# Performance work log

Hardware: AMD Instinct MI355X
Metric: run time of the kernel (lower is better)

## Reference

```python
import jax, jax.numpy as jnp
import numpy as np


def setup_inputs() -> dict:
    key = jax.random.key(0)
    k1, k2, k3, k4, k5 = jax.random.split(key, 5)
    B, Cin, H, W = 16, 64, 224, 224
    Cout, KH, KW = 64, 3, 3
    PH = PW = 32
    in_tensor = jax.random.normal(k1, (B, Cin, H, W), jnp.float32)
    weights = jax.random.normal(k2, (Cout, Cin, KH, KW), jnp.float32) * 0.05
    biases = jax.random.normal(k3, (Cout,), jnp.float32)
    # stale output buffer from a previous full conv; patch regions get overwritten
    out_tensor = jax.random.normal(k4, (B, Cout, H, W), jnp.float32)
    patch_location_tensor = jax.random.randint(k5, (B, 2), 0, H - PH, dtype=jnp.int32)
    return {
        "in_tensor": in_tensor,
        "weights": weights,
        "biases": biases,
        "out_tensor": out_tensor,
        "patch_location_tensor": patch_location_tensor,
        "padding": 1,
        "stride": 1,
        "p_height": PH,
        "p_width": PW,
        "version": 3,
    }


def reference(in_tensor, weights, biases, out_tensor, patch_location_tensor,
              padding, stride, p_height, p_width, version):
    KH, KW = weights.shape[2], weights.shape[3]
    Cin = in_tensor.shape[1]
    # pad once so output coord oy reads padded-input rows oy*stride .. oy*stride+KH-1
    xp = jnp.pad(in_tensor, ((0, 0), (0, 0), (padding, padding), (padding, padding)))
    if version in (1, 2):
        # full dense conv (versions 1/2)
        y = jax.lax.conv_general_dilated(xp, weights, (stride, stride), "VALID")
        return y + biases[None, :, None, None]
    # versions 3/4: compute conv only over the patch region, write into out buffer
    in_ph = (p_height - 1) * stride + KH  # input rows needed for PH output rows
    in_pw = (p_width - 1) * stride + KW

    def update_one(xpb, ob, loc):
        # xpb: (Cin, Hp, Wp), ob: (Cout, H, W), loc: (2,) = (y, x) in output coords
        region = jax.lax.dynamic_slice(
            xpb, (0, loc[0] * stride, loc[1] * stride), (Cin, in_ph, in_pw))
        patch = jax.lax.conv_general_dilated(
            region[None], weights, (stride, stride), "VALID")[0]
        patch = patch + biases[:, None, None]  # (Cout, PH, PW)
        return jax.lax.dynamic_update_slice(ob, patch, (0, loc[0], loc[1]))

    return jax.vmap(update_one)(xp, out_tensor, patch_location_tensor)
```

## Files before the change

### kernel.cpp

```cpp
#include <hip/hip_runtime.h>

constexpr int B_ = 16, C_ = 64, H_ = 224, W_ = 224;
constexpr int PH_ = 32, PW_ = 32;
constexpr int PLANE  = H_ * W_;
constexpr int PLANE4 = PLANE / 4;
constexpr int ROW4   = W_ / 4;
constexpr unsigned TOTAL4 = (unsigned)B_ * C_ * PLANE4;

constexpr int CONV_BLOCKS = 256;
constexpr int COPY_BLOCKS = 1792;
constexpr int THREADS = 256;

template <bool EDGE>
__device__ __forceinline__ void conv_patch(
    int b, int co0, int tid, int y, int x,
    const float* __restrict__ in, const float* __restrict__ bias,
    float* __restrict__ out, const float4* wlds)
{
    const int tx = tid & 31;
    const int ty = tid >> 5;
    const float* inb = in + (size_t)b * C_ * PLANE;

    float acc[4][4];
#pragma unroll
    for (int r = 0; r < 4; ++r)
#pragma unroll
        for (int j = 0; j < 4; ++j) acc[r][j] = 0.f;

    const int c0 = x + tx - 1;

#pragma unroll 1
    for (int cin = 0; cin < C_; ++cin) {
        const float* ip = inb + cin * PLANE;
        float4 w[9];
#pragma unroll
        for (int t = 0; t < 9; ++t) w[t] = wlds[cin * 9 + t];

#pragma unroll
        for (int r = 0; r < 4; ++r) {
            const int oy = ty + r * 8;
            const int r0 = y + oy - 1;
#pragma unroll
            for (int dy = 0; dy < 3; ++dy) {
                const int ri = r0 + dy;
                const float* rowp = ip + ri * W_;
#pragma unroll
                for (int dx = 0; dx < 3; ++dx) {
                    const int ci = c0 + dx;
                    float v;
                    if (EDGE) {
                        v = 0.f;
                        if (ri >= 0 && ci >= 0) v = rowp[ci];
                    } else {
                        v = rowp[ci];
                    }
                    const float4 wv = w[dy * 3 + dx];
                    acc[r][0] += v * wv.x;
                    acc[r][1] += v * wv.y;
                    acc[r][2] += v * wv.z;
                    acc[r][3] += v * wv.w;
                }
            }
        }
    }

    float bs[4];
#pragma unroll
    for (int j = 0; j < 4; ++j) bs[j] = bias[co0 + j];

#pragma unroll
    for (int r = 0; r < 4; ++r) {
        const int row = y + ty + r * 8;
#pragma unroll
        for (int j = 0; j < 4; ++j) {
            out[(size_t)(b * C_ + co0 + j) * PLANE + row * W_ + (x + tx)] =
                acc[r][j] + bs[j];
        }
    }
}

__global__ __launch_bounds__(THREADS) void inc_conv_fused(
    const float* __restrict__ in, const float* __restrict__ wt,
    const float* __restrict__ bias, const float* __restrict__ stale,
    const int* __restrict__ loc, float* __restrict__ out)
{
    __shared__ float4 wlds[C_ * 9];
    __shared__ int    locs[2 * B_];

    const int tid = threadIdx.x;
    const int bid = blockIdx.x;

    if (bid < CONV_BLOCKS) {
        const int b   = bid >> 4;
        const int co0 = (bid & 15) * 4;

        for (int idx = tid; idx < C_ * 9; idx += THREADS) {
            const int cin = idx / 9;
            const int tap = idx - cin * 9;
            float4 wv;
            wv.x = wt[(co0 + 0) * C_ * 9 + cin * 9 + tap];
            wv.y = wt[(co0 + 1) * C_ * 9 + cin * 9 + tap];
            wv.z = wt[(co0 + 2) * C_ * 9 + cin * 9 + tap];
            wv.w = wt[(co0 + 3) * C_ * 9 + cin * 9 + tap];
            wlds[idx] = wv;
        }
        __syncthreads();

        const int y = loc[2 * b], x = loc[2 * b + 1];
        if (y > 0 && x > 0)
            conv_patch<false>(b, co0, tid, y, x, in, bias, out, wlds);
        else
            conv_patch<true>(b, co0, tid, y, x, in, bias, out, wlds);
    } else {
        if (tid < 2 * B_) locs[tid] = loc[tid];
        __syncthreads();

        const float4* src4 = (const float4*)stale;
        float4*       dst4 = (float4*)out;
        const unsigned stride = (unsigned)COPY_BLOCKS * THREADS;
        unsigned i = (unsigned)(bid - CONV_BLOCKS) * THREADS + tid;

        for (; i < TOTAL4; i += stride) {
            const float4 v = src4[i];
            const unsigned plane = i / PLANE4;
            const unsigned p     = i - plane * PLANE4;
            const unsigned b     = plane >> 6;
            const unsigned h     = p / ROW4;
            const unsigned w4    = p - h * ROW4;
            const unsigned yy = (unsigned)locs[2 * b];
            const unsigned xx = (unsigned)locs[2 * b + 1];
            const unsigned cc0 = w4 * 4;

            const bool inrow = (h - yy) < (unsigned)PH_;
            const bool ovl = inrow & (cc0 + 3 >= xx) & (cc0 <= xx + (PW_ - 1));
            if (!ovl) {
                dst4[i] = v;
            } else {
                const float* vf = (const float*)&v;
                float* dstf = out + (size_t)i * 4;
#pragma unroll
                for (int k = 0; k < 4; ++k) {
                    const unsigned c = cc0 + k;
                    if ((c - xx) >= (unsigned)PW_) dstf[k] = vf[k];
                }
            }
        }
    }
}

extern "C" void kernel_launch(void* const* d_in, const int* in_sizes, int n_in,
                              void* d_out, int out_size, void* d_ws, size_t ws_size,
                              hipStream_t stream) {
    const float* in   = (const float*)d_in[0];
    const float* wt   = (const float*)d_in[1];
    const float* bias = (const float*)d_in[2];
    const float* st   = (const float*)d_in[3];
    const int*   loc  = (const int*)d_in[4];
    float* out = (float*)d_out;

    inc_conv_fused<<<dim3(CONV_BLOCKS + COPY_BLOCKS), dim3(THREADS), 0, stream>>>(
        in, wt, bias, st, loc, out);
}
```

Before: 514.4 us.

## Register-tile conv by 4 output columns and software-pipeline 64-byte copy chunks

```diff
diff --git a/kernel.cpp b/kernel.cpp
--- a/kernel.cpp
+++ b/kernel.cpp
@@ -3,13 +3,15 @@
 constexpr int B_ = 16, C_ = 64, H_ = 224, W_ = 224;
 constexpr int PH_ = 32, PW_ = 32;
 constexpr int PLANE  = H_ * W_;
-constexpr int PLANE4 = PLANE / 4;
-constexpr int ROW4   = W_ / 4;
-constexpr unsigned TOTAL4 = (unsigned)B_ * C_ * PLANE4;
+constexpr int GROW   = W_ / 16;
+constexpr int GPLANE = PLANE / 16;
+constexpr unsigned TOTAL16 = (unsigned)B_ * C_ * GPLANE;
 
 constexpr int CONV_BLOCKS = 256;
 constexpr int COPY_BLOCKS = 1792;
 constexpr int THREADS = 256;
+constexpr unsigned COPY_STRIDE = (unsigned)COPY_BLOCKS * THREADS;
+constexpr int COPY_ITERS = (int)(TOTAL16 / COPY_STRIDE);
 
 template <bool EDGE>
 __device__ __forceinline__ void conv_patch(
@@ -17,65 +19,71 @@
     const float* __restrict__ in, const float* __restrict__ bias,
     float* __restrict__ out, const float4* wlds)
 {
-    const int tx = tid & 31;
-    const int ty = tid >> 5;
+    const int colg = tid & 7;
+    const int oy   = tid >> 3;
+    const int ox0  = colg * 4;
     const float* inb = in + (size_t)b * C_ * PLANE;
 
     float acc[4][4];
 #pragma unroll
-    for (int r = 0; r < 4; ++r)
+    for (int k = 0; k < 4; ++k)
 #pragma unroll
-        for (int j = 0; j < 4; ++j) acc[r][j] = 0.f;
+        for (int j = 0; j < 4; ++j) acc[k][j] = 0.f;
 
-    const int c0 = x + tx - 1;
+    const int cbase = x + ox0 - 1;
+    const int rbase = y + oy - 1;
 
 #pragma unroll 1
     for (int cin = 0; cin < C_; ++cin) {
         const float* ip = inb + cin * PLANE;
+
         float4 w[9];
 #pragma unroll
         for (int t = 0; t < 9; ++t) w[t] = wlds[cin * 9 + t];
 
+        float v[3][6];
 #pragma unroll
-        for (int r = 0; r < 4; ++r) {
-            const int oy = ty + r * 8;
-            const int r0 = y + oy - 1;
+        for (int dy = 0; dy < 3; ++dy) {
+            const int ri = rbase + dy;
+            const float* rowp = ip + ri * W_;
 #pragma unroll
-            for (int dy = 0; dy < 3; ++dy) {
-                const int ri = r0 + dy;
-                const float* rowp = ip + ri * W_;
-#pragma unroll
-                for (int dx = 0; dx < 3; ++dx) {
-                    const int ci = c0 + dx;
-                    float v;
-                    if (EDGE) {
-                        v = 0.f;
-                        if (ri >= 0 && ci >= 0) v = rowp[ci];
-                    } else {
-                        v = rowp[ci];
-                    }
-                    const float4 wv = w[dy * 3 + dx];
-                    acc[r][0] += v * wv.x;
-                    acc[r][1] += v * wv.y;
-                    acc[r][2] += v * wv.z;
-                    acc[r][3] += v * wv.w;
+            for (int dx = 0; dx < 6; ++dx) {
+                const int ci = cbase + dx;
+                if (EDGE) {
+                    float t = 0.f;
+                    if (ri >= 0 && ci >= 0) t = rowp[ci];
+                    v[dy][dx] = t;
+                } else {
+                    v[dy][dx] = rowp[ci];
                 }
             }
         }
+
+#pragma unroll
+        for (int k = 0; k < 4; ++k)
+#pragma unroll
+            for (int dy = 0; dy < 3; ++dy)
+#pragma unroll
+                for (int d = 0; d < 3; ++d) {
+                    const float4 wv = w[dy * 3 + d];
+                    const float vv = v[dy][k + d];
+                    acc[k][0] += vv * wv.x;
+                    acc[k][1] += vv * wv.y;
+                    acc[k][2] += vv * wv.z;
+                    acc[k][3] += vv * wv.w;
+                }
     }
 
     float bs[4];
 #pragma unroll
     for (int j = 0; j < 4; ++j) bs[j] = bias[co0 + j];
 
+    const int orow = y + oy;
 #pragma unroll
-    for (int r = 0; r < 4; ++r) {
-        const int row = y + ty + r * 8;
+    for (int j = 0; j < 4; ++j) {
+        float* op = out + (size_t)(b * C_ + co0 + j) * PLANE + orow * W_ + (x + ox0);
 #pragma unroll
-        for (int j = 0; j < 4; ++j) {
-            out[(size_t)(b * C_ + co0 + j) * PLANE + row * W_ + (x + tx)] =
-                acc[r][j] + bs[j];
-        }
+        for (int k = 0; k < 4; ++k) op[k] = acc[k][j] + bs[j];
     }
 }
 
@@ -95,13 +103,11 @@
         const int co0 = (bid & 15) * 4;
 
         for (int idx = tid; idx < C_ * 9; idx += THREADS) {
-            const int cin = idx / 9;
-            const int tap = idx - cin * 9;
             float4 wv;
-            wv.x = wt[(co0 + 0) * C_ * 9 + cin * 9 + tap];
-            wv.y = wt[(co0 + 1) * C_ * 9 + cin * 9 + tap];
-            wv.z = wt[(co0 + 2) * C_ * 9 + cin * 9 + tap];
-            wv.w = wt[(co0 + 3) * C_ * 9 + cin * 9 + tap];
+            wv.x = wt[(co0 + 0) * C_ * 9 + idx];
+            wv.y = wt[(co0 + 1) * C_ * 9 + idx];
+            wv.z = wt[(co0 + 2) * C_ * 9 + idx];
+            wv.w = wt[(co0 + 3) * C_ * 9 + idx];
             wlds[idx] = wv;
         }
         __syncthreads();
@@ -115,35 +121,56 @@
         if (tid < 2 * B_) locs[tid] = loc[tid];
         __syncthreads();
 
-        const float4* src4 = (const float4*)stale;
-        float4*       dst4 = (float4*)out;
-        const unsigned stride = (unsigned)COPY_BLOCKS * THREADS;
+        const float4* __restrict__ src4 = (const float4*)stale;
+        float4* __restrict__ dst4 = (float4*)out;
+
         unsigned i = (unsigned)(bid - CONV_BLOCKS) * THREADS + tid;
 
-        for (; i < TOTAL4; i += stride) {
-            const float4 v = src4[i];
-            const unsigned plane = i / PLANE4;
-            const unsigned p     = i - plane * PLANE4;
+        float4 v0, v1, v2, v3;
+        {
+            const size_t q = (size_t)i * 4;
+            v0 = src4[q]; v1 = src4[q + 1]; v2 = src4[q + 2]; v3 = src4[q + 3];
+        }
+
+#pragma unroll
+        for (int it = 0; it < COPY_ITERS; ++it) {
+            const unsigned ni = i + COPY_STRIDE;
+            float4 n0, n1, n2, n3;
+            if (it < COPY_ITERS - 1) {
+                const size_t q = (size_t)ni * 4;
+                n0 = src4[q]; n1 = src4[q + 1]; n2 = src4[q + 2]; n3 = src4[q + 3];
+            } else {
+                n0 = v0; n1 = v1; n2 = v2; n3 = v3;
+            }
+
+            const unsigned plane = i / GPLANE;
+            const unsigned rem   = i - plane * GPLANE;
+            const unsigned h     = rem / GROW;
+            const unsigned c0    = (rem - h * GROW) * 16;
             const unsigned b     = plane >> 6;
-            const unsigned h     = p / ROW4;
-            const unsigned w4    = p - h * ROW4;
             const unsigned yy = (unsigned)locs[2 * b];
             const unsigned xx = (unsigned)locs[2 * b + 1];
-            const unsigned cc0 = w4 * 4;
 
             const bool inrow = (h - yy) < (unsigned)PH_;
-            const bool ovl = inrow & (cc0 + 3 >= xx) & (cc0 <= xx + (PW_ - 1));
+            const bool ovl = inrow & (c0 + 15 >= xx) & (c0 <= xx + (PW_ - 1));
+
+            const size_t q = (size_t)i * 4;
             if (!ovl) {
-                dst4[i] = v;
+                dst4[q] = v0; dst4[q + 1] = v1; dst4[q + 2] = v2; dst4[q + 3] = v3;
             } else {
-                const float* vf = (const float*)&v;
-                float* dstf = out + (size_t)i * 4;
+                const float vf[16] = {v0.x, v0.y, v0.z, v0.w,
+                                      v1.x, v1.y, v1.z, v1.w,
+                                      v2.x, v2.y, v2.z, v2.w,
+                                      v3.x, v3.y, v3.z, v3.w};
+                float* dstf = out + q * 4;
 #pragma unroll
-                for (int k = 0; k < 4; ++k) {
-                    const unsigned c = cc0 + k;
-                    if ((c - xx) >= (unsigned)PW_) dstf[k] = vf[k];
+                for (int k = 0; k < 16; ++k) {
+                    if ((c0 + k - xx) >= (unsigned)PW_) dstf[k] = vf[k];
                 }
             }
+
+            v0 = n0; v1 = n1; v2 = n2; v3 = n3;
+            i = ni;
         }
     }
 }
```

New measurement: 474.0 us. 7.9% less time.
